# Performance work log

Hardware: AMD Instinct MI355X
Metric: run time of the kernel (lower is better)

## Reference

```python
import jax, jax.numpy as jnp
import numpy as np

N = 100000   # nodes
E = 800000   # edges
NC = 500     # category nodes
EC = 20000   # category relation edges
D = 64       # out_feats
HOUR_PERIOD = 6  # emb_mix('hour') uses time_period = 6


def l2norm(x):
    # torch F.normalize(p=2, dim=-1) with eps clamp
    return x / jnp.maximum(jnp.linalg.norm(x, axis=-1, keepdims=True), 1e-12)


def proj_transh(x, norm):
    # x - <x, norm> * norm  (per-row)
    return x - jnp.sum(x * norm, axis=-1, keepdims=True) * norm


def edge_softmax(score, dst, n):
    # softmax over incoming edges of each destination node
    m = jax.ops.segment_max(score, dst, num_segments=n)
    e = jnp.exp(score - m[dst])
    s = jax.ops.segment_sum(e, dst, num_segments=n)
    return e / s[dst]


def setup_inputs() -> dict:
    key = jax.random.key(0)
    ks = jax.random.split(key, 12)
    nfeat = jax.random.normal(ks[0], (N, D), dtype=jnp.float32)
    cat_embedding = jax.random.normal(ks[1], (NC, D), dtype=jnp.float32)
    src = jax.random.randint(ks[2], (E,), 0, N, dtype=jnp.int32)
    dst = jax.random.randint(ks[3], (E,), 0, N, dtype=jnp.int32)
    feats_type = jax.random.randint(ks[4], (E,), 0, 7, dtype=jnp.int32)
    hour_id = jax.random.randint(ks[5], (E,), 0, HOUR_PERIOD, dtype=jnp.int32)
    cat_src = jax.random.randint(ks[6], (EC,), 0, NC, dtype=jnp.int32)
    cat_dst = jax.random.randint(ks[7], (EC,), 0, NC, dtype=jnp.int32)
    # learned parameters (embeddings are L2-normalized at init, as in torch code)
    rel_emb = l2norm(jax.random.normal(ks[8], (7, D), dtype=jnp.float32))
    norm_emb = l2norm(jax.random.normal(ks[9], (7, D), dtype=jnp.float32))
    hour_emb = l2norm(jax.random.normal(ks[10], (25, D), dtype=jnp.float32))
    time_rel_w = jax.random.normal(ks[11], (D, D), dtype=jnp.float32) * (1.0 / np.sqrt(D))
    time_rel_b = jnp.zeros((D,), dtype=jnp.float32)
    return {
        "nfeat": nfeat, "cat_embedding": cat_embedding,
        "rel_emb": rel_emb, "norm_emb": norm_emb, "hour_emb": hour_emb,
        "time_rel_w": time_rel_w, "time_rel_b": time_rel_b,
        "src": src, "dst": dst, "feats_type": feats_type, "hour_id": hour_id,
        "cat_src": cat_src, "cat_dst": cat_dst,
    }


def reference(nfeat, cat_embedding, rel_emb, norm_emb, hour_emb,
              time_rel_w, time_rel_b,
              src, dst, feats_type, hour_id, cat_src, cat_dst):
    # ---- category relation graph (cat_emb_type='relation', cat_score_type='transe')
    h_c = cat_embedding[cat_src]                        # [EC, D]
    t_c = cat_embedding[cat_dst]                        # [EC, D]
    rel_c = rel_emb[6]                                  # [D]
    diff_c = h_c + rel_c - t_c
    score_c = jnp.exp(-jnp.sum(diff_c * diff_c, axis=1))  # [EC]
    a_c = edge_softmax(score_c, cat_dst, NC)
    cat_hid = jax.ops.segment_sum(h_c * a_c[:, None], cat_dst, num_segments=NC)

    # ---- main graph edge features
    rel = rel_emb[feats_type]                           # [E, D]
    norm = norm_emb[feats_type]                         # [E, D]
    time_norm = norm_emb[5]                             # [D] (type-5 for all edges)
    # time relation: mixed hour embedding -> linear -> L2 normalize
    last_h = (hour_id - 1 + HOUR_PERIOD) % HOUR_PERIOD
    next_h = (hour_id + 1) % HOUR_PERIOD
    mix = (hour_emb[last_h] + hour_emb[hour_id] + hour_emb[next_h]) / 3.0  # [E, D]
    time_rel = l2norm(mix @ time_rel_w.T + time_rel_b)  # [E, D]

    h = nfeat[src]                                      # [E, D]
    t = nfeat[dst]                                      # [E, D]
    # TransH score on relation hyperplane
    d1 = proj_transh(h, norm) + rel - proj_transh(t, norm)
    score = jnp.exp(-jnp.sum(d1 * d1, axis=1))
    # TransH score on time hyperplane
    d2 = proj_transh(h, time_norm[None, :]) + time_rel - proj_transh(t, time_norm[None, :])
    score_t = jnp.exp(-jnp.sum(d2 * d2, axis=1))
    fin_score = score * score_t                         # [E]

    a = edge_softmax(fin_score, dst, N)                 # [E]
    rst = jax.ops.segment_sum(h * a[:, None], dst, num_segments=N)  # [N, D]
    return rst, cat_hid
```

## Files before the change

kernel.cpp:

```cpp
#include <hip/hip_runtime.h>

#define D 64
#define HOUR_PERIOD 6
#define CAPM 40
#define CAPC 96

__device__ __forceinline__ float bf2f(unsigned short u) {
    union { unsigned int i; float f; } v; v.i = ((unsigned int)u) << 16; return v.f;
}
__device__ __forceinline__ unsigned short f2bf(float f) {
    union { float fl; unsigned int i; } v; v.fl = f;
    unsigned int x = v.i;
    return (unsigned short)((x + 0x7fffu + ((x >> 16) & 1u)) >> 16);
}
__device__ __forceinline__ float4 ld4(const void* base, int idx4, int fp32) {
    if (fp32) return reinterpret_cast<const float4*>(base)[idx4];
    ushort4 u = reinterpret_cast<const ushort4*>(base)[idx4];
    return make_float4(bf2f(u.x), bf2f(u.y), bf2f(u.z), bf2f(u.w));
}
__device__ __forceinline__ float ld1(const void* base, int i, int fp32) {
    return fp32 ? reinterpret_cast<const float*>(base)[i]
                : bf2f(reinterpret_cast<const unsigned short*>(base)[i]);
}
__device__ __forceinline__ int detect_f(const void* rel_emb) {
    int lane = threadIdx.x & 63;
    float da = bf2f(reinterpret_cast<const unsigned short*>(rel_emb)[lane]);
    float db = bf2f(reinterpret_cast<const unsigned short*>(rel_emb)[lane + 64]);
    int bad = (!(fabsf(da) <= 100.f)) || (!(fabsf(db) <= 100.f));
    unsigned long long m = __ballot(bad);
    return (m != 0ull) ? 1 : 0;
}

template <int CTRL>
__device__ __forceinline__ float dpp_add(float v) {
    union { float f; int i; } a, b;
    a.f = v;
    b.i = __builtin_amdgcn_update_dpp(0, a.i, CTRL, 0xF, 0xF, true);
    return v + b.f;
}
__device__ __forceinline__ float qsum(float v) {
    v = dpp_add<0x128>(v);
    v = dpp_add<0x124>(v);
    v = dpp_add<0x122>(v);
    v = dpp_add<0x121>(v);
    return v;
}
__device__ __forceinline__ float wsum64(float v) {
    #pragma unroll
    for (int off = 32; off; off >>= 1) v += __shfl_xor(v, off, 64);
    return v;
}

__global__ void k_place(const int* __restrict__ src, const int* __restrict__ dst,
                        const int* __restrict__ ft, const int* __restrict__ hh,
                        const int* __restrict__ csrc, const int* __restrict__ cdst,
                        int* __restrict__ cnt, unsigned* __restrict__ recsM,
                        unsigned* __restrict__ recsC,
                        const void* __restrict__ hour_emb, const void* __restrict__ trw,
                        const void* __restrict__ trb, const void* __restrict__ rel_emb,
                        float* __restrict__ trel, int E, int EC, int N) {
    int b = blockIdx.x, t = threadIdx.x;
    if (b < HOUR_PERIOD) {
        __shared__ float mix[D];
        int f = 0;
        if (t < 64) {
            f = detect_f(rel_emb);
            int last = (b - 1 + HOUR_PERIOD) % HOUR_PERIOD;
            int next = (b + 1) % HOUR_PERIOD;
            mix[t] = (ld1(hour_emb, last * D + t, f) + ld1(hour_emb, b * D + t, f) +
                      ld1(hour_emb, next * D + t, f)) * (1.f / 3.f);
        }
        __syncthreads();
        if (t < 64) {
            float y = ld1(trb, t, f);
            #pragma unroll
            for (int k = 0; k < D; ++k) y += mix[k] * ld1(trw, t * D + k, f);
            float ss = wsum64(y * y);
            trel[b * D + t] = y / fmaxf(sqrtf(ss), 1e-12f);
        }
    }
    int tid = b * 256 + t;
    int mainT = (E + 3) >> 2;
    if (tid < mainT) {
        int e4 = tid * 4;
        if (e4 + 3 < E) {
            int4 s4 = reinterpret_cast<const int4*>(src)[tid];
            int4 d4 = reinterpret_cast<const int4*>(dst)[tid];
            int4 f4 = reinterpret_cast<const int4*>(ft)[tid];
            int4 h4 = reinterpret_cast<const int4*>(hh)[tid];
            int r0 = atomicAdd(&cnt[d4.x], 1);
            int r1 = atomicAdd(&cnt[d4.y], 1);
            int r2 = atomicAdd(&cnt[d4.z], 1);
            int r3 = atomicAdd(&cnt[d4.w], 1);
            if (r0 < CAPM) recsM[d4.x * CAPM + r0] = (unsigned)s4.x | ((unsigned)f4.x << 17) | ((unsigned)h4.x << 20);
            if (r1 < CAPM) recsM[d4.y * CAPM + r1] = (unsigned)s4.y | ((unsigned)f4.y << 17) | ((unsigned)h4.y << 20);
            if (r2 < CAPM) recsM[d4.z * CAPM + r2] = (unsigned)s4.z | ((unsigned)f4.z << 17) | ((unsigned)h4.z << 20);
            if (r3 < CAPM) recsM[d4.w * CAPM + r3] = (unsigned)s4.w | ((unsigned)f4.w << 17) | ((unsigned)h4.w << 20);
        } else {
            for (int k = e4; k < E; ++k) {
                int dv = dst[k];
                int r = atomicAdd(&cnt[dv], 1);
                if (r < CAPM)
                    recsM[dv * CAPM + r] =
                        (unsigned)src[k] | ((unsigned)ft[k] << 17) | ((unsigned)hh[k] << 20);
            }
        }
    } else {
        int j = tid - mainT, e4 = j * 4;
        if (e4 + 3 < EC) {
            int4 s4 = reinterpret_cast<const int4*>(csrc)[j];
            int4 d4 = reinterpret_cast<const int4*>(cdst)[j];
            int r0 = atomicAdd(&cnt[N + d4.x], 1);
            int r1 = atomicAdd(&cnt[N + d4.y], 1);
            int r2 = atomicAdd(&cnt[N + d4.z], 1);
            int r3 = atomicAdd(&cnt[N + d4.w], 1);
            if (r0 < CAPC) recsC[d4.x * CAPC + r0] = (unsigned)s4.x;
            if (r1 < CAPC) recsC[d4.y * CAPC + r1] = (unsigned)s4.y;
            if (r2 < CAPC) recsC[d4.z * CAPC + r2] = (unsigned)s4.z;
            if (r3 < CAPC) recsC[d4.w * CAPC + r3] = (unsigned)s4.w;
        } else {
            for (int k = e4; k < EC; ++k) {
                int dv = cdst[k];
                int r = atomicAdd(&cnt[N + dv], 1);
                if (r < CAPC) recsC[dv * CAPC + r] = (unsigned)csrc[k];
            }
        }
    }
}

__global__ __launch_bounds__(256) void k_prep(
        const void* __restrict__ nfeat, const void* __restrict__ cemb,
        const void* __restrict__ rel_emb, const void* __restrict__ norm_emb,
        const float* __restrict__ trel,
        unsigned* __restrict__ pmain, float2* __restrict__ pcat,
        float* __restrict__ consts, int N, int NC) {
    __shared__ float vt[20 * D];
    int t = threadIdx.x;
    int f = detect_f(rel_emb);
    for (int i = t; i < 7 * D; i += 256) vt[i] = ld1(rel_emb, i, f);
    for (int i = t; i < 7 * D; i += 256) vt[7 * D + i] = ld1(norm_emb, i, f);
    for (int i = t; i < 6 * D; i += 256) vt[14 * D + i] = trel[i];
    __syncthreads();
    int tid = blockIdx.x * 256 + t;
    if (tid < N) {
        float R0 = 0.f, R1 = 0.f, R2a = 0.f, R3 = 0.f, R4 = 0.f, R5 = 0.f, R6 = 0.f;
        float Nm0 = 0.f, Nm1 = 0.f, Nm2 = 0.f, Nm3 = 0.f, Nm4 = 0.f, Nm5 = 0.f, Nm6 = 0.f;
        float T0 = 0.f, T1 = 0.f, T2 = 0.f, T3 = 0.f, T4 = 0.f, T5 = 0.f;
        float S2 = 0.f;
        const float4* vp = reinterpret_cast<const float4*>(vt);
        #pragma unroll 2
        for (int k4 = 0; k4 < 16; ++k4) {
            float4 x = ld4(nfeat, tid * 16 + k4, f);
            #define DOTV(acc, v) { float4 qv = vp[(v) * 16 + k4]; \
                acc += x.x * qv.x + x.y * qv.y + x.z * qv.z + x.w * qv.w; }
            DOTV(R0, 0)  DOTV(R1, 1)  DOTV(R2a, 2) DOTV(R3, 3)
            DOTV(R4, 4)  DOTV(R5, 5)  DOTV(R6, 6)
            DOTV(Nm0, 7) DOTV(Nm1, 8) DOTV(Nm2, 9) DOTV(Nm3, 10)
            DOTV(Nm4, 11) DOTV(Nm5, 12) DOTV(Nm6, 13)
            DOTV(T0, 14) DOTV(T1, 15) DOTV(T2, 16) DOTV(T3, 17)
            DOTV(T4, 18) DOTV(T5, 19)
            #undef DOTV
            S2 += x.x * x.x + x.y * x.y + x.z * x.z + x.w * x.w;
        }
        unsigned w0 = (unsigned)f2bf(Nm0) | ((unsigned)f2bf(R0) << 16);
        unsigned w1 = (unsigned)f2bf(Nm1) | ((unsigned)f2bf(R1) << 16);
        unsigned w2 = (unsigned)f2bf(Nm2) | ((unsigned)f2bf(R2a) << 16);
        unsigned w3 = (unsigned)f2bf(Nm3) | ((unsigned)f2bf(R3) << 16);
        unsigned w4 = (unsigned)f2bf(Nm4) | ((unsigned)f2bf(R4) << 16);
        unsigned w5 = (unsigned)f2bf(Nm5) | ((unsigned)f2bf(R5) << 16);
        unsigned w6 = (unsigned)f2bf(Nm6) | ((unsigned)f2bf(R6) << 16);
        unsigned w7 = (unsigned)f2bf(T0) | ((unsigned)f2bf(T1) << 16);
        unsigned w8 = (unsigned)f2bf(T2) | ((unsigned)f2bf(T3) << 16);
        unsigned w9 = (unsigned)f2bf(T4) | ((unsigned)f2bf(T5) << 16);
        union { float ff; unsigned u; } cs, ca;
        cs.ff = S2; ca.ff = Nm5;
        uint4* dp = reinterpret_cast<uint4*>(pmain + (size_t)tid * 16);
        dp[0] = make_uint4(w0, w1, w2, w3);
        dp[1] = make_uint4(w4, w5, w6, w7);
        dp[2] = make_uint4(w8, w9, cs.u, ca.u);
        dp[3] = make_uint4(0, 0, 0, 0);
    } else if (tid - N < NC) {
        int i = tid - N;
        float S = 0.f, Cr = 0.f;
        #pragma unroll 4
        for (int k4 = 0; k4 < 16; ++k4) {
            float4 x = ld4(cemb, i * 16 + k4, f);
            float4 rv = *reinterpret_cast<const float4*>(&vt[6 * D + k4 * 4]);
            S  += x.x * x.x + x.y * x.y + x.z * x.z + x.w * x.w;
            Cr += x.x * rv.x + x.y * rv.y + x.z * rv.z + x.w * rv.w;
        }
        pcat[i] = make_float2(S, Cr);
    }
    if (blockIdx.x == 0) {
        if (t < 7) {
            float R2 = 0.f, RN = 0.f, N2 = 0.f;
            for (int k = 0; k < D; ++k) {
                float r = vt[t * D + k], n = vt[(7 + t) * D + k];
                R2 += r * r; RN += r * n; N2 += n * n;
            }
            consts[t * 4 + 0] = R2; consts[t * 4 + 1] = RN;
            consts[t * 4 + 2] = N2 - 2.f; consts[t * 4 + 3] = 0.f;
        } else if (t < 13) {
            int hv = t - 7;
            float T2c = 0.f, TQ = 0.f;
            for (int k = 0; k < D; ++k) {
                float a = vt[(14 + hv) * D + k], qv = vt[12 * D + k];
                T2c += a * a; TQ += a * qv;
            }
            consts[28 + hv * 2] = T2c; consts[29 + hv * 2] = TQ;
        } else if (t == 13) {
            float Q2 = 0.f;
            for (int k = 0; k < D; ++k) { float qv = vt[12 * D + k]; Q2 += qv * qv; }
            consts[40] = Q2 - 2.f;
        } else if (t == 14) {
            float R = 0.f;
            for (int k = 0; k < D; ++k) { float r = vt[6 * D + k]; R += r * r; }
            consts[41] = R;
        }
    }
}

__launch_bounds__(256, 6)
__global__ void k_fused(const void* __restrict__ nfeat, const void* __restrict__ cemb,
                        const void* __restrict__ rel_emb,
                        const unsigned char* __restrict__ pmain,
                        const float2* __restrict__ pcat,
                        const float* __restrict__ consts,
                        const int* __restrict__ cnt,
                        const unsigned* __restrict__ recsM,
                        const unsigned* __restrict__ recsC,
                        void* __restrict__ out, int N, int M) {
    int t = threadIdx.x;
    int f = detect_f(rel_emb);
    __shared__ __align__(16) float sc[44];
    if (t < 42) sc[t] = consts[t];
    __syncthreads();
    int lane = t & 63, w = t >> 6;
    int l = lane & 15, q = lane >> 4;
    float Q2m2 = sc[40], R2c = sc[41];
    int dbase = (blockIdx.x * 4 + w) * 4;
    for (int d = dbase; d < dbase + 4 && d < M; ++d) {
        float a0 = 0.f, a1 = 0.f, a2 = 0.f, a3 = 0.f, se = 0.f;
        if (d < N) {
            int nE = cnt[d]; nE = nE > CAPM ? CAPM : nE;
            int i0 = d * CAPM, i1 = i0 + nE;
            float4 tt = ld4(nfeat, d * 16 + l, f);
            const unsigned char* pd = pmain + (size_t)d * 64;
            float2 sd2 = *reinterpret_cast<const float2*>(pd + 40);
            int i = i0 + q;
            unsigned pkA = 0, awsA = 0, awdA = 0;
            unsigned short dhsA = 0, dhdA = 0;
            float2 saA = make_float2(0.f, 0.f);
            float4 hA = make_float4(0.f, 0.f, 0.f, 0.f);
            if (i < i1) {
                pkA = recsM[i];
                int s = pkA & 0x1FFFF, fv = (pkA >> 17) & 7, hv = (pkA >> 20) & 7;
                const unsigned char* ps = pmain + (size_t)s * 64;
                hA = ld4(nfeat, s * 16 + l, f);
                awsA = *reinterpret_cast<const unsigned*>(ps + 4 * fv);
                dhsA = *reinterpret_cast<const unsigned short*>(ps + 28 + 2 * hv);
                saA  = *reinterpret_cast<const float2*>(ps + 40);
                awdA = *reinterpret_cast<const unsigned*>(pd + 4 * fv);
                dhdA = *reinterpret_cast<const unsigned short*>(pd + 28 + 2 * hv);
            }
            for (; i < i1; i += 4) {
                unsigned cpk = pkA, caws = awsA, cawd = awdA;
                unsigned short cdhs = dhsA, cdhd = dhdA;
                float2 csa = saA; float4 ch = hA;
                if (i + 4 < i1) {
                    pkA = recsM[i + 4];
                    int s = pkA & 0x1FFFF, fv = (pkA >> 17) & 7, hv = (pkA >> 20) & 7;
                    const unsigned char* ps = pmain + (size_t)s * 64;
                    hA = ld4(nfeat, s * 16 + l, f);
                    awsA = *reinterpret_cast<const unsigned*>(ps + 4 * fv);
                    dhsA = *reinterpret_cast<const unsigned short*>(ps + 28 + 2 * hv);
                    saA  = *reinterpret_cast<const float2*>(ps + 40);
                    awdA = *reinterpret_cast<const unsigned*>(pd + 4 * fv);
                    dhdA = *reinterpret_cast<const unsigned short*>(pd + 28 + 2 * hv);
                }
                int fv = (cpk >> 17) & 7, hv = (cpk >> 20) & 7;
                float4 cf  = *reinterpret_cast<float4*>(&sc[fv * 4]);
                float2 cth = *reinterpret_cast<float2*>(&sc[28 + hv * 2]);
                float hdot = qsum(ch.x * tt.x + ch.y * tt.y + ch.z * tt.z + ch.w * tt.w);
                float As = bf2f((unsigned short)(caws & 0xFFFFu));
                float Cs = bf2f((unsigned short)(caws >> 16));
                float Ad = bf2f((unsigned short)(cawd & 0xFFFFu));
                float Cd = bf2f((unsigned short)(cawd >> 16));
                float Dhs = bf2f(cdhs), Dhd = bf2f(cdhd);
                float al = As - Ad;
                float be = csa.y - sd2.y;
                float w2 = csa.x + sd2.x - 2.f * hdot;
                float ssq = 2.f * w2 + cf.x + cth.x + 2.f * (Cs - Cd) + 2.f * (Dhs - Dhd)
                          + al * al * cf.z - 2.f * al * cf.y
                          + be * be * Q2m2 - 2.f * be * cth.y;
                float es = __expf(__expf(-ssq));
                a0 += es * ch.x; a1 += es * ch.y; a2 += es * ch.z; a3 += es * ch.w;
                se += es;
            }
        } else {
            int dc = d - N;
            int nE = cnt[d]; nE = nE > CAPC ? CAPC : nE;
            int i0 = dc * CAPC, i1 = i0 + nE;
            float4 tt = ld4(cemb, dc * 16 + l, f);
            float2 td = pcat[dc];
            int i = i0 + q;
            unsigned pkA = 0;
            float4 hA = make_float4(0.f, 0.f, 0.f, 0.f);
            float2 shA = make_float2(0.f, 0.f);
            if (i < i1) {
                pkA = recsC[i];
                hA = ld4(cemb, (int)pkA * 16 + l, f);
                shA = pcat[pkA];
            }
            for (; i < i1; i += 4) {
                float4 ch = hA; float2 csh = shA;
                if (i + 4 < i1) {
                    pkA = recsC[i + 4];
                    hA = ld4(cemb, (int)pkA * 16 + l, f);
                    shA = pcat[pkA];
                }
                float hdot = qsum(ch.x * tt.x + ch.y * tt.y + ch.z * tt.z + ch.w * tt.w);
                float ssq = csh.x + td.x + R2c + 2.f * csh.y - 2.f * td.y - 2.f * hdot;
                float es = __expf(__expf(-ssq));
                a0 += es * ch.x; a1 += es * ch.y; a2 += es * ch.z; a3 += es * ch.w;
                se += es;
            }
        }
        a0 += __shfl_xor(a0, 16, 64); a0 += __shfl_xor(a0, 32, 64);
        a1 += __shfl_xor(a1, 16, 64); a1 += __shfl_xor(a1, 32, 64);
        a2 += __shfl_xor(a2, 16, 64); a2 += __shfl_xor(a2, 32, 64);
        a3 += __shfl_xor(a3, 16, 64); a3 += __shfl_xor(a3, 32, 64);
        se += __shfl_xor(se, 16, 64); se += __shfl_xor(se, 32, 64);
        float inv = (se > 0.f) ? 1.f / se : 0.f;
        if (q == 0) {
            int oi = d * 16 + l;
            if (f) {
                reinterpret_cast<float4*>(out)[oi] =
                    make_float4(a0 * inv, a1 * inv, a2 * inv, a3 * inv);
            } else {
                ushort4 o;
                o.x = f2bf(a0 * inv); o.y = f2bf(a1 * inv);
                o.z = f2bf(a2 * inv); o.w = f2bf(a3 * inv);
                reinterpret_cast<ushort4*>(out)[oi] = o;
            }
        }
    }
}

extern "C" void kernel_launch(void* const* d_in, const int* in_sizes, int n_in,
                              void* d_out, int out_size, void* d_ws, size_t ws_size,
                              hipStream_t stream) {
    const void* nfeat    = d_in[0];
    const void* cemb     = d_in[1];
    const void* rel_emb  = d_in[2];
    const void* norm_emb = d_in[3];
    const void* hour_emb = d_in[4];
    const void* trw      = d_in[5];
    const void* trb      = d_in[6];
    const int* src    = (const int*)d_in[7];
    const int* dst    = (const int*)d_in[8];
    const int* ftype  = (const int*)d_in[9];
    const int* hourid = (const int*)d_in[10];
    const int* csrc   = (const int*)d_in[11];
    const int* cdst   = (const int*)d_in[12];

    const int N  = in_sizes[0] / D;
    const int NC = in_sizes[1] / D;
    const int E  = in_sizes[7];
    const int EC = in_sizes[11];
    const int M  = N + NC;

    unsigned char* base = (unsigned char*)d_ws;
    size_t o = 0;
    int* cnt = (int*)(base + o);          o += ((size_t)M * 4 + 255) & ~(size_t)255;
    float* trel = (float*)(base + o);     o += ((size_t)HOUR_PERIOD * D * 4 + 255) & ~(size_t)255;
    float* consts = (float*)(base + o);   o += 256;
    unsigned* pmain = (unsigned*)(base + o); o += (size_t)N * 64;
    float2* pcat = (float2*)(base + o);   o += ((size_t)NC * 8 + 255) & ~(size_t)255;
    unsigned* recsM = (unsigned*)(base + o); o += (size_t)N * CAPM * 4;
    unsigned* recsC = (unsigned*)(base + o); o += (size_t)NC * CAPC * 4;

    (void)hipMemsetAsync(cnt, 0, (size_t)M * 4, stream);

    int histT = (E + 3) / 4 + (EC + 3) / 4;
    int gplace = (histT + 255) / 256;
    if (gplace < HOUR_PERIOD) gplace = HOUR_PERIOD;
    k_place<<<gplace, 256, 0, stream>>>(src, dst, ftype, hourid, csrc, cdst,
                                        cnt, recsM, recsC,
                                        hour_emb, trw, trb, rel_emb, trel, E, EC, N);
    int gprep = (M + 255) / 256;
    k_prep<<<gprep, 256, 0, stream>>>(nfeat, cemb, rel_emb, norm_emb, trel,
                                      pmain, pcat, consts, N, NC);
    k_fused<<<(M + 15) / 16, 256, 0, stream>>>(nfeat, cemb, rel_emb,
                                               (const unsigned char*)pmain, pcat,
                                               consts, cnt,
                                               recsM, recsC, d_out, N, M);
}
```

Before: 243.4 us.

## Merge edge placement and node prep kernels, pad counters, use 8-lane edge groups

Merges the edge-bucketing kernel and the per-node projection prep kernel into one launch, with disjoint block ranges, so they run concurrently. Each prep block now recomputes the small time-relation table (mixed hour embedding through the linear layer) itself. Per-destination counters are padded to a stride of 8 ints to reduce atomic contention on shared cache lines. The gather kernel switches from 16 lanes × 4 features with a 4-edge software prefetch to 8 lanes × 8 features processing 8 edges per step, with fewer reduction steps; launch bounds are relaxed from 6 to 4 waves. The cost is redundant tiny matmuls per prep block, a larger counter memset, and possibly lower occupancy.

```diff
diff --git a/kernel.cpp b/kernel.cpp
--- a/kernel.cpp
+++ b/kernel.cpp
@@ -4,6 +4,7 @@
 #define HOUR_PERIOD 6
 #define CAPM 40
 #define CAPC 96
+#define CSTR 8
 
 __device__ __forceinline__ float bf2f(unsigned short u) {
     union { unsigned int i; float f; } v; v.i = ((unsigned int)u) << 16; return v.f;
@@ -21,6 +22,22 @@
 __device__ __forceinline__ float ld1(const void* base, int i, int fp32) {
     return fp32 ? reinterpret_cast<const float*>(base)[i]
                 : bf2f(reinterpret_cast<const unsigned short*>(base)[i]);
+}
+__device__ __forceinline__ void ld8(const void* base, int row, int l, int f,
+                                    float& h0, float& h1, float& h2, float& h3,
+                                    float& h4, float& h5, float& h6, float& h7) {
+    if (f) {
+        const float4* p = reinterpret_cast<const float4*>(base) + row * 16 + l * 2;
+        float4 u = p[0], v = p[1];
+        h0 = u.x; h1 = u.y; h2 = u.z; h3 = u.w;
+        h4 = v.x; h5 = v.y; h6 = v.z; h7 = v.w;
+    } else {
+        uint4 u = reinterpret_cast<const uint4*>(base)[row * 8 + l];
+        h0 = bf2f((unsigned short)(u.x & 0xFFFFu)); h1 = bf2f((unsigned short)(u.x >> 16));
+        h2 = bf2f((unsigned short)(u.y & 0xFFFFu)); h3 = bf2f((unsigned short)(u.y >> 16));
+        h4 = bf2f((unsigned short)(u.z & 0xFFFFu)); h5 = bf2f((unsigned short)(u.z >> 16));
+        h6 = bf2f((unsigned short)(u.w & 0xFFFFu)); h7 = bf2f((unsigned short)(u.w >> 16));
+    }
 }
 __device__ __forceinline__ int detect_f(const void* rel_emb) {
     int lane = threadIdx.x & 63;
@@ -30,118 +47,107 @@
     unsigned long long m = __ballot(bad);
     return (m != 0ull) ? 1 : 0;
 }
-
-template <int CTRL>
-__device__ __forceinline__ float dpp_add(float v) {
-    union { float f; int i; } a, b;
-    a.f = v;
-    b.i = __builtin_amdgcn_update_dpp(0, a.i, CTRL, 0xF, 0xF, true);
-    return v + b.f;
-}
-__device__ __forceinline__ float qsum(float v) {
-    v = dpp_add<0x128>(v);
-    v = dpp_add<0x124>(v);
-    v = dpp_add<0x122>(v);
-    v = dpp_add<0x121>(v);
-    return v;
-}
 __device__ __forceinline__ float wsum64(float v) {
     #pragma unroll
     for (int off = 32; off; off >>= 1) v += __shfl_xor(v, off, 64);
     return v;
 }
-
-__global__ void k_place(const int* __restrict__ src, const int* __restrict__ dst,
-                        const int* __restrict__ ft, const int* __restrict__ hh,
-                        const int* __restrict__ csrc, const int* __restrict__ cdst,
-                        int* __restrict__ cnt, unsigned* __restrict__ recsM,
-                        unsigned* __restrict__ recsC,
-                        const void* __restrict__ hour_emb, const void* __restrict__ trw,
-                        const void* __restrict__ trb, const void* __restrict__ rel_emb,
-                        float* __restrict__ trel, int E, int EC, int N) {
-    int b = blockIdx.x, t = threadIdx.x;
-    if (b < HOUR_PERIOD) {
-        __shared__ float mix[D];
-        int f = 0;
-        if (t < 64) {
-            f = detect_f(rel_emb);
-            int last = (b - 1 + HOUR_PERIOD) % HOUR_PERIOD;
-            int next = (b + 1) % HOUR_PERIOD;
-            mix[t] = (ld1(hour_emb, last * D + t, f) + ld1(hour_emb, b * D + t, f) +
-                      ld1(hour_emb, next * D + t, f)) * (1.f / 3.f);
-        }
-        __syncthreads();
-        if (t < 64) {
-            float y = ld1(trb, t, f);
-            #pragma unroll
-            for (int k = 0; k < D; ++k) y += mix[k] * ld1(trw, t * D + k, f);
-            float ss = wsum64(y * y);
-            trel[b * D + t] = y / fmaxf(sqrtf(ss), 1e-12f);
-        }
-    }
-    int tid = b * 256 + t;
-    int mainT = (E + 3) >> 2;
-    if (tid < mainT) {
-        int e4 = tid * 4;
-        if (e4 + 3 < E) {
-            int4 s4 = reinterpret_cast<const int4*>(src)[tid];
-            int4 d4 = reinterpret_cast<const int4*>(dst)[tid];
-            int4 f4 = reinterpret_cast<const int4*>(ft)[tid];
-            int4 h4 = reinterpret_cast<const int4*>(hh)[tid];
-            int r0 = atomicAdd(&cnt[d4.x], 1);
-            int r1 = atomicAdd(&cnt[d4.y], 1);
-            int r2 = atomicAdd(&cnt[d4.z], 1);
-            int r3 = atomicAdd(&cnt[d4.w], 1);
-            if (r0 < CAPM) recsM[d4.x * CAPM + r0] = (unsigned)s4.x | ((unsigned)f4.x << 17) | ((unsigned)h4.x << 20);
-            if (r1 < CAPM) recsM[d4.y * CAPM + r1] = (unsigned)s4.y | ((unsigned)f4.y << 17) | ((unsigned)h4.y << 20);
-            if (r2 < CAPM) recsM[d4.z * CAPM + r2] = (unsigned)s4.z | ((unsigned)f4.z << 17) | ((unsigned)h4.z << 20);
-            if (r3 < CAPM) recsM[d4.w * CAPM + r3] = (unsigned)s4.w | ((unsigned)f4.w << 17) | ((unsigned)h4.w << 20);
+__device__ __forceinline__ float rsum8(float v) {
+    v += __shfl_xor(v, 1, 64);
+    v += __shfl_xor(v, 2, 64);
+    v += __shfl_xor(v, 4, 64);
+    return v;
+}
+
+__global__ void k_pp(const int* __restrict__ src, const int* __restrict__ dst,
+                     const int* __restrict__ ft, const int* __restrict__ hh,
+                     const int* __restrict__ csrc, const int* __restrict__ cdst,
+                     int* __restrict__ cnt, unsigned* __restrict__ recsM,
+                     unsigned* __restrict__ recsC,
+                     const void* __restrict__ nfeat, const void* __restrict__ cemb,
+                     const void* __restrict__ rel_emb, const void* __restrict__ norm_emb,
+                     const void* __restrict__ hour_emb, const void* __restrict__ trw,
+                     const void* __restrict__ trb,
+                     unsigned* __restrict__ pmain, float2* __restrict__ pcat,
+                     float* __restrict__ consts,
+                     int E, int EC, int N, int NC, int GP) {
+    __shared__ float vt[20 * D];
+    __shared__ float mix6[HOUR_PERIOD * D];
+    __shared__ float trwT[D * 65];
+    int t = threadIdx.x;
+    if (blockIdx.x < GP) {
+        int tid = blockIdx.x * 256 + t;
+        int mainT = (E + 3) >> 2;
+        if (tid < mainT) {
+            int e4 = tid * 4;
+            if (e4 + 3 < E) {
+                int4 s4 = reinterpret_cast<const int4*>(src)[tid];
+                int4 d4 = reinterpret_cast<const int4*>(dst)[tid];
+                int4 f4 = reinterpret_cast<const int4*>(ft)[tid];
+                int4 h4 = reinterpret_cast<const int4*>(hh)[tid];
+                int r0 = atomicAdd(&cnt[d4.x * CSTR], 1);
+                int r1 = atomicAdd(&cnt[d4.y * CSTR], 1);
+                int r2 = atomicAdd(&cnt[d4.z * CSTR], 1);
+                int r3 = atomicAdd(&cnt[d4.w * CSTR], 1);
+                if (r0 < CAPM) recsM[d4.x * CAPM + r0] = (unsigned)s4.x | ((unsigned)f4.x << 17) | ((unsigned)h4.x << 20);
+                if (r1 < CAPM) recsM[d4.y * CAPM + r1] = (unsigned)s4.y | ((unsigned)f4.y << 17) | ((unsigned)h4.y << 20);
+                if (r2 < CAPM) recsM[d4.z * CAPM + r2] = (unsigned)s4.z | ((unsigned)f4.z << 17) | ((unsigned)h4.z << 20);
+                if (r3 < CAPM) recsM[d4.w * CAPM + r3] = (unsigned)s4.w | ((unsigned)f4.w << 17) | ((unsigned)h4.w << 20);
+            } else {
+                for (int k = e4; k < E; ++k) {
+                    int dv = dst[k];
+                    int r = atomicAdd(&cnt[dv * CSTR], 1);
+                    if (r < CAPM)
+                        recsM[dv * CAPM + r] =
+                            (unsigned)src[k] | ((unsigned)ft[k] << 17) | ((unsigned)hh[k] << 20);
+                }
+            }
         } else {
-            for (int k = e4; k < E; ++k) {
-                int dv = dst[k];
-                int r = atomicAdd(&cnt[dv], 1);
-                if (r < CAPM)
-                    recsM[dv * CAPM + r] =
-                        (unsigned)src[k] | ((unsigned)ft[k] << 17) | ((unsigned)hh[k] << 20);
-            }
-        }
-    } else {
-        int j = tid - mainT, e4 = j * 4;
-        if (e4 + 3 < EC) {
-            int4 s4 = reinterpret_cast<const int4*>(csrc)[j];
-            int4 d4 = reinterpret_cast<const int4*>(cdst)[j];
-            int r0 = atomicAdd(&cnt[N + d4.x], 1);
-            int r1 = atomicAdd(&cnt[N + d4.y], 1);
-            int r2 = atomicAdd(&cnt[N + d4.z], 1);
-            int r3 = atomicAdd(&cnt[N + d4.w], 1);
-            if (r0 < CAPC) recsC[d4.x * CAPC + r0] = (unsigned)s4.x;
-            if (r1 < CAPC) recsC[d4.y * CAPC + r1] = (unsigned)s4.y;
-            if (r2 < CAPC) recsC[d4.z * CAPC + r2] = (unsigned)s4.z;
-            if (r3 < CAPC) recsC[d4.w * CAPC + r3] = (unsigned)s4.w;
-        } else {
-            for (int k = e4; k < EC; ++k) {
-                int dv = cdst[k];
-                int r = atomicAdd(&cnt[N + dv], 1);
-                if (r < CAPC) recsC[dv * CAPC + r] = (unsigned)csrc[k];
-            }
-        }
-    }
-}
-
-__global__ __launch_bounds__(256) void k_prep(
-        const void* __restrict__ nfeat, const void* __restrict__ cemb,
-        const void* __restrict__ rel_emb, const void* __restrict__ norm_emb,
-        const float* __restrict__ trel,
-        unsigned* __restrict__ pmain, float2* __restrict__ pcat,
-        float* __restrict__ consts, int N, int NC) {
-    __shared__ float vt[20 * D];
-    int t = threadIdx.x;
+            int j = tid - mainT, e4 = j * 4;
+            if (e4 + 3 < EC) {
+                int4 s4 = reinterpret_cast<const int4*>(csrc)[j];
+                int4 d4 = reinterpret_cast<const int4*>(cdst)[j];
+                int r0 = atomicAdd(&cnt[(N + d4.x) * CSTR], 1);
+                int r1 = atomicAdd(&cnt[(N + d4.y) * CSTR], 1);
+                int r2 = atomicAdd(&cnt[(N + d4.z) * CSTR], 1);
+                int r3 = atomicAdd(&cnt[(N + d4.w) * CSTR], 1);
+                if (r0 < CAPC) recsC[d4.x * CAPC + r0] = (unsigned)s4.x;
+                if (r1 < CAPC) recsC[d4.y * CAPC + r1] = (unsigned)s4.y;
+                if (r2 < CAPC) recsC[d4.z * CAPC + r2] = (unsigned)s4.z;
+                if (r3 < CAPC) recsC[d4.w * CAPC + r3] = (unsigned)s4.w;
+            } else {
+                for (int k = e4; k < EC; ++k) {
+                    int dv = cdst[k];
+                    int r = atomicAdd(&cnt[(N + dv) * CSTR], 1);
+                    if (r < CAPC) recsC[dv * CAPC + r] = (unsigned)csrc[k];
+                }
+            }
+        }
+        return;
+    }
+    int pb = blockIdx.x - GP;
     int f = detect_f(rel_emb);
+    int lane = t & 63, w = t >> 6;
     for (int i = t; i < 7 * D; i += 256) vt[i] = ld1(rel_emb, i, f);
     for (int i = t; i < 7 * D; i += 256) vt[7 * D + i] = ld1(norm_emb, i, f);
-    for (int i = t; i < 6 * D; i += 256) vt[14 * D + i] = trel[i];
+    for (int i = t; i < HOUR_PERIOD * D; i += 256) {
+        int hv = i >> 6, k = i & 63;
+        int last = (hv + HOUR_PERIOD - 1) % HOUR_PERIOD, next = (hv + 1) % HOUR_PERIOD;
+        mix6[i] = (ld1(hour_emb, last * D + k, f) + ld1(hour_emb, hv * D + k, f) +
+                   ld1(hour_emb, next * D + k, f)) * (1.f / 3.f);
+    }
+    for (int i = t; i < D * D; i += 256)
+        trwT[(i & 63) * 65 + (i >> 6)] = ld1(trw, i, f);
     __syncthreads();
-    int tid = blockIdx.x * 256 + t;
+    for (int hv = w; hv < HOUR_PERIOD; hv += 4) {
+        float y = ld1(trb, lane, f);
+        #pragma unroll 4
+        for (int kk = 0; kk < D; ++kk) y += mix6[hv * D + kk] * trwT[kk * 65 + lane];
+        float ss = wsum64(y * y);
+        vt[(14 + hv) * D + lane] = y / fmaxf(sqrtf(ss), 1e-12f);
+    }
+    __syncthreads();
+    int tid = pb * 256 + t;
     if (tid < N) {
         float R0 = 0.f, R1 = 0.f, R2a = 0.f, R3 = 0.f, R4 = 0.f, R5 = 0.f, R6 = 0.f;
         float Nm0 = 0.f, Nm1 = 0.f, Nm2 = 0.f, Nm3 = 0.f, Nm4 = 0.f, Nm5 = 0.f, Nm6 = 0.f;
@@ -191,7 +197,7 @@
         }
         pcat[i] = make_float2(S, Cr);
     }
-    if (blockIdx.x == 0) {
+    if (pb == 0) {
         if (t < 7) {
             float R2 = 0.f, RN = 0.f, N2 = 0.f;
             for (int k = 0; k < D; ++k) {
@@ -220,7 +226,7 @@
     }
 }
 
-__launch_bounds__(256, 6)
+__launch_bounds__(256, 4)
 __global__ void k_fused(const void* __restrict__ nfeat, const void* __restrict__ cemb,
                         const void* __restrict__ rel_emb,
                         const unsigned char* __restrict__ pmain,
@@ -236,112 +242,98 @@
     if (t < 42) sc[t] = consts[t];
     __syncthreads();
     int lane = t & 63, w = t >> 6;
-    int l = lane & 15, q = lane >> 4;
+    int l = lane & 7, q = lane >> 3;
     float Q2m2 = sc[40], R2c = sc[41];
     int dbase = (blockIdx.x * 4 + w) * 4;
     for (int d = dbase; d < dbase + 4 && d < M; ++d) {
-        float a0 = 0.f, a1 = 0.f, a2 = 0.f, a3 = 0.f, se = 0.f;
+        float a0 = 0.f, a1 = 0.f, a2 = 0.f, a3 = 0.f;
+        float a4 = 0.f, a5 = 0.f, a6 = 0.f, a7 = 0.f, se = 0.f;
         if (d < N) {
-            int nE = cnt[d]; nE = nE > CAPM ? CAPM : nE;
-            int i0 = d * CAPM, i1 = i0 + nE;
-            float4 tt = ld4(nfeat, d * 16 + l, f);
+            int nE = cnt[d * CSTR]; nE = nE > CAPM ? CAPM : nE;
+            int i0 = d * CAPM;
+            float t0, t1, t2, t3, t4, t5, t6, t7;
+            ld8(nfeat, d, l, f, t0, t1, t2, t3, t4, t5, t6, t7);
             const unsigned char* pd = pmain + (size_t)d * 64;
             float2 sd2 = *reinterpret_cast<const float2*>(pd + 40);
-            int i = i0 + q;
-            unsigned pkA = 0, awsA = 0, awdA = 0;
-            unsigned short dhsA = 0, dhdA = 0;
-            float2 saA = make_float2(0.f, 0.f);
-            float4 hA = make_float4(0.f, 0.f, 0.f, 0.f);
-            if (i < i1) {
-                pkA = recsM[i];
-                int s = pkA & 0x1FFFF, fv = (pkA >> 17) & 7, hv = (pkA >> 20) & 7;
+            unsigned pk = (nE > 0) ? recsM[i0 + q] : 0u;
+            for (int b = 0; b < nE; b += 8) {
+                unsigned pkn = 0u;
+                if (b + 8 < nE) pkn = recsM[i0 + b + 8 + q];
+                int valid = (b + q) < nE;
+                unsigned pkv = valid ? pk : 0u;
+                int s = pkv & 0x1FFFF, fv = (pkv >> 17) & 7, hv = (pkv >> 20) & 7;
                 const unsigned char* ps = pmain + (size_t)s * 64;
-                hA = ld4(nfeat, s * 16 + l, f);
-                awsA = *reinterpret_cast<const unsigned*>(ps + 4 * fv);
-                dhsA = *reinterpret_cast<const unsigned short*>(ps + 28 + 2 * hv);
-                saA  = *reinterpret_cast<const float2*>(ps + 40);
-                awdA = *reinterpret_cast<const unsigned*>(pd + 4 * fv);
-                dhdA = *reinterpret_cast<const unsigned short*>(pd + 28 + 2 * hv);
-            }
-            for (; i < i1; i += 4) {
-                unsigned cpk = pkA, caws = awsA, cawd = awdA;
-                unsigned short cdhs = dhsA, cdhd = dhdA;
-                float2 csa = saA; float4 ch = hA;
-                if (i + 4 < i1) {
-                    pkA = recsM[i + 4];
-                    int s = pkA & 0x1FFFF, fv = (pkA >> 17) & 7, hv = (pkA >> 20) & 7;
-                    const unsigned char* ps = pmain + (size_t)s * 64;
-                    hA = ld4(nfeat, s * 16 + l, f);
-                    awsA = *reinterpret_cast<const unsigned*>(ps + 4 * fv);
-                    dhsA = *reinterpret_cast<const unsigned short*>(ps + 28 + 2 * hv);
-                    saA  = *reinterpret_cast<const float2*>(ps + 40);
-                    awdA = *reinterpret_cast<const unsigned*>(pd + 4 * fv);
-                    dhdA = *reinterpret_cast<const unsigned short*>(pd + 28 + 2 * hv);
-                }
-                int fv = (cpk >> 17) & 7, hv = (cpk >> 20) & 7;
+                float h0, h1, h2, h3, h4, h5, h6, h7;
+                ld8(nfeat, s, l, f, h0, h1, h2, h3, h4, h5, h6, h7);
+                unsigned aws = *reinterpret_cast<const unsigned*>(ps + 4 * fv);
+                unsigned short dhs = *reinterpret_cast<const unsigned short*>(ps + 28 + 2 * hv);
+                float2 sa = *reinterpret_cast<const float2*>(ps + 40);
+                unsigned awd = *reinterpret_cast<const unsigned*>(pd + 4 * fv);
+                unsigned short dhd = *reinterpret_cast<const unsigned short*>(pd + 28 + 2 * hv);
                 float4 cf  = *reinterpret_cast<float4*>(&sc[fv * 4]);
                 float2 cth = *reinterpret_cast<float2*>(&sc[28 + hv * 2]);
-                float hdot = qsum(ch.x * tt.x + ch.y * tt.y + ch.z * tt.z + ch.w * tt.w);
-                float As = bf2f((unsigned short)(caws & 0xFFFFu));
-                float Cs = bf2f((unsigned short)(caws >> 16));
-                float Ad = bf2f((unsigned short)(cawd & 0xFFFFu));
-                float Cd = bf2f((unsigned short)(cawd >> 16));
-                float Dhs = bf2f(cdhs), Dhd = bf2f(cdhd);
+                float hdot = rsum8(h0 * t0 + h1 * t1 + h2 * t2 + h3 * t3 +
+                                   h4 * t4 + h5 * t5 + h6 * t6 + h7 * t7);
+                float As = bf2f((unsigned short)(aws & 0xFFFFu));
+                float Cs = bf2f((unsigned short)(aws >> 16));
+                float Ad = bf2f((unsigned short)(awd & 0xFFFFu));
+                float Cd = bf2f((unsigned short)(awd >> 16));
+                float Dhs = bf2f(dhs), Dhd = bf2f(dhd);
                 float al = As - Ad;
-                float be = csa.y - sd2.y;
-                float w2 = csa.x + sd2.x - 2.f * hdot;
+                float be = sa.y - sd2.y;
+                float w2 = sa.x + sd2.x - 2.f * hdot;
                 float ssq = 2.f * w2 + cf.x + cth.x + 2.f * (Cs - Cd) + 2.f * (Dhs - Dhd)
                           + al * al * cf.z - 2.f * al * cf.y
                           + be * be * Q2m2 - 2.f * be * cth.y;
                 float es = __expf(__expf(-ssq));
-                a0 += es * ch.x; a1 += es * ch.y; a2 += es * ch.z; a3 += es * ch.w;
+                es = valid ? es : 0.f;
+                a0 += es * h0; a1 += es * h1; a2 += es * h2; a3 += es * h3;
+                a4 += es * h4; a5 += es * h5; a6 += es * h6; a7 += es * h7;
                 se += es;
+                pk = pkn;
             }
         } else {
             int dc = d - N;
-            int nE = cnt[d]; nE = nE > CAPC ? CAPC : nE;
-            int i0 = dc * CAPC, i1 = i0 + nE;
-            float4 tt = ld4(cemb, dc * 16 + l, f);
+            int nE = cnt[d * CSTR]; nE = nE > CAPC ? CAPC : nE;
+            int i0 = dc * CAPC;
+            float t0, t1, t2, t3, t4, t5, t6, t7;
+            ld8(cemb, dc, l, f, t0, t1, t2, t3, t4, t5, t6, t7);
             float2 td = pcat[dc];
-            int i = i0 + q;
-            unsigned pkA = 0;
-            float4 hA = make_float4(0.f, 0.f, 0.f, 0.f);
-            float2 shA = make_float2(0.f, 0.f);
-            if (i < i1) {
-                pkA = recsC[i];
-                hA = ld4(cemb, (int)pkA * 16 + l, f);
-                shA = pcat[pkA];
-            }
-            for (; i < i1; i += 4) {
-                float4 ch = hA; float2 csh = shA;
-                if (i + 4 < i1) {
-                    pkA = recsC[i + 4];
-                    hA = ld4(cemb, (int)pkA * 16 + l, f);
-                    shA = pcat[pkA];
-                }
-                float hdot = qsum(ch.x * tt.x + ch.y * tt.y + ch.z * tt.z + ch.w * tt.w);
+            unsigned pk = (nE > 0) ? recsC[i0 + q] : 0u;
+            for (int b = 0; b < nE; b += 8) {
+                unsigned pkn = 0u;
+                if (b + 8 < nE) pkn = recsC[i0 + b + 8 + q];
+                int valid = (b + q) < nE;
+                unsigned s = valid ? pk : 0u;
+                float h0, h1, h2, h3, h4, h5, h6, h7;
+                ld8(cemb, (int)s, l, f, h0, h1, h2, h3, h4, h5, h6, h7);
+                float2 csh = pcat[s];
+                float hdot = rsum8(h0 * t0 + h1 * t1 + h2 * t2 + h3 * t3 +
+                                   h4 * t4 + h5 * t5 + h6 * t6 + h7 * t7);
                 float ssq = csh.x + td.x + R2c + 2.f * csh.y - 2.f * td.y - 2.f * hdot;
                 float es = __expf(__expf(-ssq));
-                a0 += es * ch.x; a1 += es * ch.y; a2 += es * ch.z; a3 += es * ch.w;
+                es = valid ? es : 0.f;
+                a0 += es * h0; a1 += es * h1; a2 += es * h2; a3 += es * h3;
+                a4 += es * h4; a5 += es * h5; a6 += es * h6; a7 += es * h7;
                 se += es;
-            }
-        }
-        a0 += __shfl_xor(a0, 16, 64); a0 += __shfl_xor(a0, 32, 64);
-        a1 += __shfl_xor(a1, 16, 64); a1 += __shfl_xor(a1, 32, 64);
-        a2 += __shfl_xor(a2, 16, 64); a2 += __shfl_xor(a2, 32, 64);
-        a3 += __shfl_xor(a3, 16, 64); a3 += __shfl_xor(a3, 32, 64);
-        se += __shfl_xor(se, 16, 64); se += __shfl_xor(se, 32, 64);
+                pk = pkn;
+            }
+        }
+        #define RED(x) x += __shfl_xor(x, 8, 64); x += __shfl_xor(x, 16, 64); x += __shfl_xor(x, 32, 64);
+        RED(a0) RED(a1) RED(a2) RED(a3) RED(a4) RED(a5) RED(a6) RED(a7) RED(se)
+        #undef RED
         float inv = (se > 0.f) ? 1.f / se : 0.f;
         if (q == 0) {
-            int oi = d * 16 + l;
             if (f) {
-                reinterpret_cast<float4*>(out)[oi] =
-                    make_float4(a0 * inv, a1 * inv, a2 * inv, a3 * inv);
+                float4* op = reinterpret_cast<float4*>(out) + d * 16 + l * 2;
+                op[0] = make_float4(a0 * inv, a1 * inv, a2 * inv, a3 * inv);
+                op[1] = make_float4(a4 * inv, a5 * inv, a6 * inv, a7 * inv);
             } else {
-                ushort4 o;
-                o.x = f2bf(a0 * inv); o.y = f2bf(a1 * inv);
-                o.z = f2bf(a2 * inv); o.w = f2bf(a3 * inv);
-                reinterpret_cast<ushort4*>(out)[oi] = o;
+                unsigned w0 = (unsigned)f2bf(a0 * inv) | ((unsigned)f2bf(a1 * inv) << 16);
+                unsigned w1 = (unsigned)f2bf(a2 * inv) | ((unsigned)f2bf(a3 * inv) << 16);
+                unsigned w2 = (unsigned)f2bf(a4 * inv) | ((unsigned)f2bf(a5 * inv) << 16);
+                unsigned w3 = (unsigned)f2bf(a6 * inv) | ((unsigned)f2bf(a7 * inv) << 16);
+                reinterpret_cast<uint4*>(out)[d * 8 + l] = make_uint4(w0, w1, w2, w3);
             }
         }
     }
@@ -372,25 +364,24 @@
 
     unsigned char* base = (unsigned char*)d_ws;
     size_t o = 0;
-    int* cnt = (int*)(base + o);          o += ((size_t)M * 4 + 255) & ~(size_t)255;
-    float* trel = (float*)(base + o);     o += ((size_t)HOUR_PERIOD * D * 4 + 255) & ~(size_t)255;
+    int* cnt = (int*)(base + o);          o += ((size_t)M * CSTR * 4 + 255) & ~(size_t)255;
     float* consts = (float*)(base + o);   o += 256;
     unsigned* pmain = (unsigned*)(base + o); o += (size_t)N * 64;
     float2* pcat = (float2*)(base + o);   o += ((size_t)NC * 8 + 255) & ~(size_t)255;
     unsigned* recsM = (unsigned*)(base + o); o += (size_t)N * CAPM * 4;
     unsigned* recsC = (unsigned*)(base + o); o += (size_t)NC * CAPC * 4;
 
-    (void)hipMemsetAsync(cnt, 0, (size_t)M * 4, stream);
+    (void)hipMemsetAsync(cnt, 0, (size_t)M * CSTR * 4, stream);
 
     int histT = (E + 3) / 4 + (EC + 3) / 4;
-    int gplace = (histT + 255) / 256;
-    if (gplace < HOUR_PERIOD) gplace = HOUR_PERIOD;
-    k_place<<<gplace, 256, 0, stream>>>(src, dst, ftype, hourid, csrc, cdst,
-                                        cnt, recsM, recsC,
-                                        hour_emb, trw, trb, rel_emb, trel, E, EC, N);
-    int gprep = (M + 255) / 256;
-    k_prep<<<gprep, 256, 0, stream>>>(nfeat, cemb, rel_emb, norm_emb, trel,
-                                      pmain, pcat, consts, N, NC);
+    int GP    = (histT + 255) / 256;
+    int GPREP = (M + 255) / 256;
+    k_pp<<<GP + GPREP, 256, 0, stream>>>(src, dst, ftype, hourid, csrc, cdst,
+                                         cnt, recsM, recsC,
+                                         nfeat, cemb, rel_emb, norm_emb,
+                                         hour_emb, trw, trb,
+                                         pmain, pcat, consts,
+                                         E, EC, N, NC, GP);
     k_fused<<<(M + 15) / 16, 256, 0, stream>>>(nfeat, cemb, rel_emb,
                                                (const unsigned char*)pmain, pcat,
                                                consts, cnt,
```

Result: no change. 239.1 us (-1.8%).
